# Performance work log

Measured on AMD Instinct MI355X. Metric: run time of the kernel, lower is better.

Reference implementation:

```python
import jax, jax.numpy as jnp
import numpy as np
from jax.scipy.special import logsumexp

B, S, H, L = 64, 512, 1024, 9  # batch, seq_len, hidden_size, num_labels


def setup_inputs() -> dict:
    key = jax.random.key(0)
    ks = jax.random.split(key, 6)
    inputs = jax.random.normal(ks[0], (B, S, H), jnp.float32)
    labels = jax.random.randint(ks[1], (B, S), 0, L).astype(jnp.int64)
    mask = jnp.ones((B, S), jnp.int32)
    # fc parameters (nn.Linear(hidden_size, num_labels))
    W = jax.random.normal(ks[2], (L, H), jnp.float32) / np.sqrt(H)
    b = jnp.zeros((L,), jnp.float32)
    # CRF parameters (include_start_end_trans=True)
    trans_m = jax.random.normal(ks[3], (L, L), jnp.float32) * 0.1
    start_scores = jax.random.normal(ks[4], (L,), jnp.float32) * 0.1
    end_scores = jax.random.normal(ks[5], (L,), jnp.float32) * 0.1
    return dict(inputs=inputs, labels=labels, mask=mask, W=W, b=b,
                trans_m=trans_m, start_scores=start_scores, end_scores=end_scores)


def _crf_nll_mean(inputs, W, b, trans_m, start_scores, end_scores, labels, mask):
    # logits = fc(inputs): [B, S, L]
    logits = jnp.einsum('bsh,lh->bsl', inputs, W) + b
    feats = jnp.swapaxes(logits, 0, 1)           # [S, B, L] (fastNLP transposes)
    tags = jnp.swapaxes(labels, 0, 1)            # [S, B]
    m = jnp.swapaxes(mask, 0, 1).astype(feats.dtype)  # [S, B]
    seq_len, batch, n_tags = feats.shape

    # ---- log-partition via forward algorithm (lax.scan over time) ----
    alpha0 = feats[0] + start_scores[None, :]    # [B, L]

    def step(alpha, x):
        emit, mt = x                              # emit: [B, L], mt: [B]
        # tmp[b, i, j] = alpha[b, i] + trans_m[i, j] + emit[b, j]
        tmp = alpha[:, :, None] + trans_m[None, :, :] + emit[:, None, :]
        new = logsumexp(tmp, axis=1)              # [B, L]
        alpha = jnp.where(mt[:, None] > 0, new, alpha)
        return alpha, None

    alpha, _ = jax.lax.scan(step, alpha0, (feats[1:], m[1:]))
    norm = logsumexp(alpha + end_scores[None, :], axis=1)   # [B]

    # ---- gold path score ----
    emit = jnp.take_along_axis(feats, tags[:, :, None], axis=2)[:, :, 0] * m  # [S, B]
    trans = trans_m[tags[:-1], tags[1:]] * m[1:]                               # [S-1, B]
    score = emit.sum(0) + trans.sum(0)                                         # [B]
    last_idx = m.sum(0).astype(jnp.int32) - 1                                  # [B]
    last_tags = tags[last_idx, jnp.arange(batch)]
    score = score + start_scores[tags[0]] + end_scores[last_tags]

    # loss = crf(logits, labels, mask).mean()
    return jnp.mean(norm - score)


def reference(inputs, labels, mask, W, b, trans_m, start_scores, end_scores):
    return _crf_nll_mean(inputs, W, b, trans_m, start_scores, end_scores, labels, mask)
```

## Files before the change

kernel.cpp:

```cpp
#include <hip/hip_runtime.h>


#define BATCH 64
#define SEQ   512
#define HID   1024
#define NLAB  9
#define CHUNK 32
#define NCHUNK (SEQ / CHUNK)
#define NREC (BATCH * NCHUNK * NLAB)

__device__ __forceinline__ float exp2_fast(float x) { return __builtin_amdgcn_exp2f(x); }
__device__ __forceinline__ float log2_fast(float x) { return __builtin_amdgcn_logf(x); }

#define LOG2E 1.4426950408889634f
#define LN2   0.6931471805599453f

__global__ __launch_bounds__(256) void logits_kernel(
    const float* __restrict__ inp, const float* __restrict__ Wg,
    const float* __restrict__ bias, float* __restrict__ feats)
{
    __shared__ float Wl[NLAB * 1056];
    const int tid = threadIdx.x;
    for (int i = tid; i < NLAB * HID; i += 256) {
        int l = i >> 10, col = i & 1023;
        Wl[l * 1056 + col + (col >> 5)] = Wg[i];
    }
    __syncthreads();

    const int lane = tid & 63;
    const int wv = tid >> 6;
    const long row0 = (long)blockIdx.x * 8 + wv * 2;
    const int col0 = lane * 16;
    const int sk = col0 + (col0 >> 5);

    float xs0[16], xs1[16];
    {
        const float* r0 = inp + row0 * HID + col0;
        const float* r1 = r0 + HID;
        #pragma unroll
        for (int q = 0; q < 4; ++q) {
            ((float4*)xs0)[q] = ((const float4*)r0)[q];
            ((float4*)xs1)[q] = ((const float4*)r1)[q];
        }
    }

    float acc0[NLAB], acc1[NLAB];
    #pragma unroll
    for (int l = 0; l < NLAB; ++l) {
        const float* w = &Wl[l * 1056 + sk];
        float a0 = 0.f, a1 = 0.f;
        #pragma unroll
        for (int k = 0; k < 16; ++k) {
            float wk = w[k];
            a0 = fmaf(xs0[k], wk, a0);
            a1 = fmaf(xs1[k], wk, a1);
        }
        acc0[l] = a0; acc1[l] = a1;
    }
    #pragma unroll
    for (int l = 0; l < NLAB; ++l) {
        float a0 = acc0[l], a1 = acc1[l];
        #pragma unroll
        for (int off = 32; off > 0; off >>= 1) {
            a0 += __shfl_xor(a0, off, 64);
            a1 += __shfl_xor(a1, off, 64);
        }
        acc0[l] = a0; acc1[l] = a1;
    }
    if (lane == 0) {
        float* o = feats + row0 * NLAB;
        #pragma unroll
        for (int l = 0; l < NLAB; ++l) {
            float bl = bias[l];
            o[l]        = (acc0[l] + bl) * LOG2E;
            o[NLAB + l] = (acc1[l] + bl) * LOG2E;
        }
    }
}

__global__ __launch_bounds__(64) void chunk_kernel(
    const float* __restrict__ feats, const float* __restrict__ trans,
    const int* __restrict__ mask, float* __restrict__ P)
{
    const int lane = threadIdx.x;
    const int g = lane / 9;
    const int j = lane - g * 9;
    int rid = blockIdx.x * 7 + g;
    bool act = (g < 7) && (rid < NREC);
    if (!act) rid = 0;

    const int i  = rid % NLAB;
    const int bc = rid / NLAB;
    const int c  = bc & (NCHUNK - 1);
    const int b  = bc >> 4;

    float tr[NLAB];
    #pragma unroll
    for (int k = 0; k < NLAB; ++k) tr[k] = trans[k * NLAB + j] * LOG2E;
    const float tri = trans[i * NLAB + j] * LOG2E;

    const float* fb = feats + (long)b * SEQ * NLAB;
    const int* mb = mask + b * SEQ;
    const int ts = (c == 0) ? 1 : c * CHUNK;
    const int te = (c + 1) * CHUNK;
    const int sbase = g * 9;

    float a;
    {
        int m0 = mb[ts];
        float e0 = fb[ts * NLAB + j];
        float aid = (i == j) ? 0.0f : -1e30f;
        a = (m0 > 0) ? (tri + e0) : aid;
    }

    float e_nxt = fb[(ts + 1) * NLAB + j];
    int   m_nxt = mb[ts + 1];
    for (int t = ts + 1; t < te; ++t) {
        float e = e_nxt;
        int  mt = m_nxt;
        if (t + 1 < te) {
            e_nxt = fb[(t + 1) * NLAB + j];
            m_nxt = mb[t + 1];
        }
        float v[NLAB];
        #pragma unroll
        for (int k = 0; k < NLAB; ++k) v[k] = __shfl(a, sbase + k, 64) + tr[k];
        float m01 = fmaxf(v[0], v[1]), m23 = fmaxf(v[2], v[3]);
        float m45 = fmaxf(v[4], v[5]), m67 = fmaxf(v[6], v[7]);
        float mx = fmaxf(fmaxf(fmaxf(m01, m23), fmaxf(m45, m67)), v[8]);
        float s = 0.0f;
        #pragma unroll
        for (int k = 0; k < NLAB; ++k) s += exp2_fast(v[k] - mx);
        float an = mx + log2_fast(s) + e;
        a = (mt > 0) ? an : a;
    }
    if (act) P[(long)rid * NLAB + j] = a;
}

__global__ __launch_bounds__(64) void final_kernel(
    const float* __restrict__ feats, const float* __restrict__ trans,
    const float* __restrict__ startv, const float* __restrict__ endv,
    const int* __restrict__ labels, const int* __restrict__ mask,
    const float* __restrict__ P, float* __restrict__ partial)
{
    const int b = blockIdx.x, lane = threadIdx.x;
    const float* fb = feats + (long)b * SEQ * NLAB;
    const int* lb = labels + b * SEQ;
    const int* mb = mask + b * SEQ;

    float gsum = 0.0f; int msum = 0;
    for (int t = lane; t < SEQ; t += 64) {
        int tag = lb[t];
        int mt = mb[t];
        if (mt > 0) {
            gsum += fb[t * NLAB + tag];
            msum++;
            if (t > 0) gsum += trans[lb[t - 1] * NLAB + tag] * LOG2E;
        }
    }
    #pragma unroll
    for (int off = 32; off > 0; off >>= 1) {
        gsum += __shfl_xor(gsum, off, 64);
        msum += __shfl_xor(msum, off, 64);
    }

    const int j = lane % 9;
    float al = fb[j] + startv[j] * LOG2E;
    const float* Pb = P + (long)b * NCHUNK * 81;
    float pc[NLAB];
    #pragma unroll
    for (int i = 0; i < NLAB; ++i) pc[i] = Pb[i * NLAB + j];
    #pragma unroll
    for (int c = 0; c < NCHUNK; ++c) {
        float pn[NLAB];
        if (c < NCHUNK - 1) {
            #pragma unroll
            for (int i = 0; i < NLAB; ++i) pn[i] = Pb[(c + 1) * 81 + i * NLAB + j];
        } else {
            #pragma unroll
            for (int i = 0; i < NLAB; ++i) pn[i] = 0.0f;
        }
        float v[NLAB];
        #pragma unroll
        for (int i = 0; i < NLAB; ++i) v[i] = __shfl(al, i, 64) + pc[i];
        float m01 = fmaxf(v[0], v[1]), m23 = fmaxf(v[2], v[3]);
        float m45 = fmaxf(v[4], v[5]), m67 = fmaxf(v[6], v[7]);
        float mx = fmaxf(fmaxf(fmaxf(m01, m23), fmaxf(m45, m67)), v[8]);
        float s = 0.0f;
        #pragma unroll
        for (int i = 0; i < NLAB; ++i) s += exp2_fast(v[i] - mx);
        al = mx + log2_fast(s);
        #pragma unroll
        for (int i = 0; i < NLAB; ++i) pc[i] = pn[i];
    }
    al += endv[j] * LOG2E;

    float v[NLAB];
    #pragma unroll
    for (int i = 0; i < NLAB; ++i) v[i] = __shfl(al, i, 64);
    float m01 = fmaxf(v[0], v[1]), m23 = fmaxf(v[2], v[3]);
    float m45 = fmaxf(v[4], v[5]), m67 = fmaxf(v[6], v[7]);
    float mx = fmaxf(fmaxf(fmaxf(m01, m23), fmaxf(m45, m67)), v[8]);
    float s = 0.0f;
    #pragma unroll
    for (int i = 0; i < NLAB; ++i) s += exp2_fast(v[i] - mx);
    float norm = mx + log2_fast(s);

    if (lane == 0) {
        int li = (msum > 0) ? (msum - 1) : 0;
        float score = gsum + startv[lb[0]] * LOG2E + endv[lb[li]] * LOG2E;
        partial[b] = norm - score;
    }
}

__global__ __launch_bounds__(64) void mean_kernel(
    const float* __restrict__ partial, float* __restrict__ out)
{
    float v = partial[threadIdx.x];
    #pragma unroll
    for (int off = 32; off > 0; off >>= 1) v += __shfl_xor(v, off, 64);
    if (threadIdx.x == 0) out[0] = v * (LN2 / (float)BATCH);
}

extern "C" void kernel_launch(void* const* d_in, const int* in_sizes, int n_in,
                              void* d_out, int out_size, void* d_ws, size_t ws_size,
                              hipStream_t stream)
{
    const float* inp    = (const float*)d_in[0];
    const int*   labels = (const int*)d_in[1];
    const int*   mask   = (const int*)d_in[2];
    const float* W      = (const float*)d_in[3];
    const float* bias   = (const float*)d_in[4];
    const float* trans  = (const float*)d_in[5];
    const float* startv = (const float*)d_in[6];
    const float* endv   = (const float*)d_in[7];

    float* feats   = (float*)d_ws;
    float* P       = feats + BATCH * SEQ * NLAB;
    float* partial = P + BATCH * NCHUNK * 81;
    float* out = (float*)d_out;

    hipLaunchKernelGGL(logits_kernel, dim3(BATCH * SEQ / 8), dim3(256), 0, stream,
                       inp, W, bias, feats);
    hipLaunchKernelGGL(chunk_kernel, dim3((NREC + 6) / 7), dim3(64), 0, stream,
                       feats, trans, mask, P);
    hipLaunchKernelGGL(final_kernel, dim3(BATCH), dim3(64), 0, stream,
                       feats, trans, startv, endv, labels, mask, P, partial);
    hipLaunchKernelGGL(mean_kernel, dim3(1), dim3(64), 0, stream, partial, out);
}
```

Measured before the change: 246.5 us.

## Process 16 rows per block with 16-lane row groups in logits GEMV

Result: faster. 235.2 us (-4.6%).

```diff
diff --git a/kernel.cpp b/kernel.cpp
--- a/kernel.cpp
+++ b/kernel.cpp
@@ -28,53 +28,48 @@
     __syncthreads();
 
     const int lane = tid & 63;
-    const int wv = tid >> 6;
-    const long row0 = (long)blockIdx.x * 8 + wv * 2;
-    const int col0 = lane * 16;
-    const int sk = col0 + (col0 >> 5);
-
-    float xs0[16], xs1[16];
-    {
-        const float* r0 = inp + row0 * HID + col0;
-        const float* r1 = r0 + HID;
-        #pragma unroll
-        for (int q = 0; q < 4; ++q) {
-            ((float4*)xs0)[q] = ((const float4*)r0)[q];
-            ((float4*)xs1)[q] = ((const float4*)r1)[q];
-        }
-    }
-
-    float acc0[NLAB], acc1[NLAB];
+    const int wv   = tid >> 6;
+    const int p    = lane & 15;
+    const int q    = lane >> 4;
+    const long row = (long)blockIdx.x * 16 + wv * 4 + q;
+
+    const float* r = inp + row * HID;
+    float acc[NLAB];
+    #pragma unroll
+    for (int l = 0; l < NLAB; ++l) acc[l] = 0.f;
+
+    #pragma unroll
+    for (int c = 0; c < 4; ++c) {
+        const int col0 = c * 256 + p * 16;
+        float xs[16];
+        #pragma unroll
+        for (int qq = 0; qq < 4; ++qq)
+            ((float4*)xs)[qq] = ((const float4*)(r + col0))[qq];
+        const int sk = col0 + (col0 >> 5);
+        #pragma unroll
+        for (int l = 0; l < NLAB; ++l) {
+            const float* w = &Wl[l * 1056 + sk];
+            float a = acc[l];
+            #pragma unroll
+            for (int k = 0; k < 16; ++k) a = fmaf(xs[k], w[k], a);
+            acc[l] = a;
+        }
+    }
+
     #pragma unroll
     for (int l = 0; l < NLAB; ++l) {
-        const float* w = &Wl[l * 1056 + sk];
-        float a0 = 0.f, a1 = 0.f;
-        #pragma unroll
-        for (int k = 0; k < 16; ++k) {
-            float wk = w[k];
-            a0 = fmaf(xs0[k], wk, a0);
-            a1 = fmaf(xs1[k], wk, a1);
-        }
-        acc0[l] = a0; acc1[l] = a1;
-    }
-    #pragma unroll
-    for (int l = 0; l < NLAB; ++l) {
-        float a0 = acc0[l], a1 = acc1[l];
-        #pragma unroll
-        for (int off = 32; off > 0; off >>= 1) {
-            a0 += __shfl_xor(a0, off, 64);
-            a1 += __shfl_xor(a1, off, 64);
-        }
-        acc0[l] = a0; acc1[l] = a1;
-    }
-    if (lane == 0) {
-        float* o = feats + row0 * NLAB;
-        #pragma unroll
-        for (int l = 0; l < NLAB; ++l) {
-            float bl = bias[l];
-            o[l]        = (acc0[l] + bl) * LOG2E;
-            o[NLAB + l] = (acc1[l] + bl) * LOG2E;
-        }
+        float a = acc[l];
+        a += __shfl_xor(a, 8, 64);
+        a += __shfl_xor(a, 4, 64);
+        a += __shfl_xor(a, 2, 64);
+        a += __shfl_xor(a, 1, 64);
+        acc[l] = a;
+    }
+    if (p == 0) {
+        float* o = feats + row * NLAB;
+        #pragma unroll
+        for (int l = 0; l < NLAB; ++l)
+            o[l] = (acc[l] + bias[l]) * LOG2E;
     }
 }
 
@@ -240,7 +235,7 @@
     float* partial = P + BATCH * NCHUNK * 81;
     float* out = (float*)d_out;
 
-    hipLaunchKernelGGL(logits_kernel, dim3(BATCH * SEQ / 8), dim3(256), 0, stream,
+    hipLaunchKernelGGL(logits_kernel, dim3(BATCH * SEQ / 16), dim3(256), 0, stream,
                        inp, W, bias, feats);
     hipLaunchKernelGGL(chunk_kernel, dim3((NREC + 6) / 7), dim3(64), 0, stream,
                        feats, trans, mask, P);
```
